# Kernel tuning notes

Hardware: AMD Instinct MI355X
Metric: run time of the kernel (lower is better)

Reference implementation:

```python
import jax, jax.numpy as jnp
from jax import lax
import numpy as np

B, L1, L2 = 64, 1024, 1024


def setup_inputs() -> dict:
    key = jax.random.key(0)
    ks = jax.random.split(key, 6)
    s1 = 1.0 / np.sqrt(L1)
    s2 = 1.0 / np.sqrt(L2)
    return {
        "a": jax.random.normal(ks[0], (B, L1), dtype=jnp.float32),
        "b": jax.random.normal(ks[1], (B, L2), dtype=jnp.float32),
        # nn.Linear(L1, L1) and nn.Linear(L2, L2) params (PyTorch default uniform init range)
        "W1": jax.random.uniform(ks[2], (L1, L1), jnp.float32, -s1, s1),
        "b1": jax.random.uniform(ks[3], (L1,), jnp.float32, -s1, s1),
        "W2": jax.random.uniform(ks[4], (L2, L2), jnp.float32, -s2, s2),
        "b2": jax.random.uniform(ks[5], (L2,), jnp.float32, -s2, s2),
    }


def _dtw_cost(cost):
    """DTW accumulated-cost DP for one [N, M] pairwise-cost matrix.

    R[i,j] = cost[i,j] + min(R[i-1,j-1], R[i-1,j], R[i,j-1]).
    The within-row dependency x[j] = c[j] + min(m[j], x[j-1]) is a min-plus
    prefix: x[j] = S[j] + cummin(m - S_{j-1}) with S = cumsum(c), which lets
    each row be computed in parallel (wavefront-equivalent vectorization).
    Returns the scalar DTW distance R[N-1, M-1].
    """
    dt = cost.dtype
    row0 = jnp.cumsum(cost[0])  # R[0, :]

    def step(prev_row, c_row):
        # m[j] = min(R[i-1, j], R[i-1, j-1]);  j=0 has no (i-1, j-1) neighbor
        shifted = jnp.concatenate([jnp.full((1,), jnp.inf, dt), prev_row[:-1]])
        m = jnp.minimum(prev_row, shifted)
        S = jnp.cumsum(c_row)
        S_prev = jnp.concatenate([jnp.zeros((1,), dt), S[:-1]])
        row = S + lax.associative_scan(jnp.minimum, m - S_prev)
        return row, None

    last_row, _ = lax.scan(step, row0, cost[1:])
    return last_row[-1]


def reference(a, b, W1, b1, W2, b2):
    # seq1 / seq2 linear projections over the time axis
    a_p = a @ W1.T + b1  # [B, L1]
    b_p = b @ W2.T + b2  # [B, L2]
    # squared-euclidean pairwise cost (scipy.sqeuclidean on scalar elements)
    cost = (a_p[:, :, None] - b_p[:, None, :]) ** 2  # [B, L1, L2]
    return jax.vmap(_dtw_cost)(cost)  # [B] DTW distances
```

## Files before the change

kernel.cpp:

```cpp
#include <hip/hip_runtime.h>
#include <math.h>


#define L 1024
#define BATCH 64

__global__ __launch_bounds__(256) void proj_kernel(
    const float* __restrict__ a, const float* __restrict__ b,
    const float* __restrict__ W1, const float* __restrict__ b1,
    const float* __restrict__ W2, const float* __restrict__ b2,
    float* __restrict__ ap, float* __restrict__ bp, int KC) {
  int part = blockIdx.x >> 7;
  int sub = blockIdx.x & 127;
  const float* X;
  const float* W;
  const float* bias;
  float* out;
  int i0;
  if (sub < 64) {
    X = a; W = W1; bias = b1; out = ap + part * BATCH * L; i0 = sub * 16;
  } else {
    X = b; W = W2; bias = b2; out = bp + part * BATCH * L; i0 = (sub - 64) * 16;
  }

  __shared__ float a_s[64][33];
  __shared__ float w_s[16][33];

  int tid = threadIdx.x;
  int lane_b = tid & 63;
  int iq = tid >> 6;

  float acc[4] = {0.f, 0.f, 0.f, 0.f};

  int kbeg = part * KC;
  int kend = kbeg + KC;
  for (int k0 = kbeg; k0 < kend; k0 += 32) {
    {
      int row = tid >> 2;
      int kl = (tid & 3) * 8;
      const float4* src = reinterpret_cast<const float4*>(&X[row * L + k0 + kl]);
      float4 v0 = src[0];
      float4 v1 = src[1];
      a_s[row][kl + 0] = v0.x; a_s[row][kl + 1] = v0.y;
      a_s[row][kl + 2] = v0.z; a_s[row][kl + 3] = v0.w;
      a_s[row][kl + 4] = v1.x; a_s[row][kl + 5] = v1.y;
      a_s[row][kl + 6] = v1.z; a_s[row][kl + 7] = v1.w;
    }
    {
      int row = tid >> 4;
      int kl = (tid & 15) * 2;
      float2 v = *reinterpret_cast<const float2*>(&W[(i0 + row) * L + k0 + kl]);
      w_s[row][kl] = v.x;
      w_s[row][kl + 1] = v.y;
    }
    __syncthreads();
    #pragma unroll 8
    for (int kl = 0; kl < 32; ++kl) {
      float av = a_s[lane_b][kl];
      #pragma unroll
      for (int m = 0; m < 4; ++m) {
        acc[m] += av * w_s[iq * 4 + m][kl];
      }
    }
    __syncthreads();
  }

  #pragma unroll
  for (int m = 0; m < 4; ++m) {
    int i = i0 + iq * 4 + m;
    float bv = (part == 0) ? bias[i] : 0.f;
    out[lane_b * L + i] = acc[m] + bv;
  }
}


#define NW 4
#define CPL 4
#define KBAR 32
#define OFF 95
#define DMAX (OFF * (NW - 1) + 63)
#define NG 43
#define NSTEPS (NG * KBAR)
#define APPAD (DMAX + NSTEPS + 64)

__device__ __forceinline__ float dpp_shr1(float v, float old) {
  int r = __builtin_amdgcn_update_dpp(__float_as_int(old), __float_as_int(v),
                                      0x138, 0xf, 0xf, false);
  return __int_as_float(r);
}

__device__ __forceinline__ float dpp_shl1(float v) {
  int r = __builtin_amdgcn_update_dpp(__float_as_int(v), __float_as_int(v),
                                      0x130, 0xf, 0xf, false);
  return __int_as_float(r);
}

__device__ __forceinline__ float min3f(float x, float y, float z) {
  float r;
  asm("v_min3_f32 %0, %1, %2, %3" : "=v"(r) : "v"(x), "v"(y), "v"(z));
  return r;
}

__global__ __launch_bounds__(256) void dtw_kernel(const float* __restrict__ app,
                                                  const float* __restrict__ bpp,
                                                  float* __restrict__ out,
                                                  int parts) {
  const int b = blockIdx.x;
  const int tid = threadIdx.x;
  const int w = tid >> 6;
  const int t = tid & 63;
  const int woff = w * OFF;
  const int D = woff + t;
  const float INF = INFINITY;

  __shared__ float ap_pad[APPAD];
  __shared__ float ring[NW - 1][64];

  for (int idx = tid; idx < APPAD; idx += 256) {
    int src = idx - DMAX;
    float v = 0.f;
    if ((unsigned)src < (unsigned)L) {
      v = app[b * L + src];
      for (int p = 1; p < parts; ++p) v += app[p * BATCH * L + b * L + src];
    }
    ap_pad[idx] = v;
  }

  float4 bv = *reinterpret_cast<const float4*>(&bpp[b * L + tid * CPL]);
  for (int p = 1; p < parts; ++p) {
    float4 u = *reinterpret_cast<const float4*>(
        &bpp[p * BATCH * L + b * L + tid * CPL]);
    bv.x += u.x; bv.y += u.y; bv.z += u.z; bv.w += u.w;
  }
  const float bpv0 = bv.x, bpv1 = bv.y, bpv2 = bv.z, bpv3 = bv.w;

  float p0 = INF, p1 = INF, p2 = INF, p3 = INF;
  float right = INF, prev_left = INF, apv = 0.f;
  float ringchunk = (w == 0 && t == 0) ? 0.f : INF;
  float apchunk = 0.f;
  float vprod = INF;
  const int ap_base = DMAX - woff + t;

  __syncthreads();

#define STEP_CORE()                                                          \
    float dprev = prev_left;                                                 \
    prev_left = left;                                                        \
    float d0 = apv - bpv0, d1 = apv - bpv1, d2 = apv - bpv2, d3 = apv - bpv3;\
    float x = left, bb;                                                      \
    bb = min3f(p0, dprev, x); x = __builtin_fmaf(d0, d0, bb); dprev = p0; p0 = x; \
    bb = min3f(p1, dprev, x); x = __builtin_fmaf(d1, d1, bb); dprev = p1; p1 = x; \
    bb = min3f(p2, dprev, x); x = __builtin_fmaf(d2, d2, bb); dprev = p2; p2 = x; \
    bb = min3f(p3, dprev, x); x = __builtin_fmaf(d3, d3, bb); p3 = x;        \
    right = x;

#define STEP_FAST()                                                          \
  {                                                                          \
    float left = dpp_shr1(right, ringchunk);                                 \
    apv = dpp_shr1(apv, apchunk);                                            \
    apchunk = dpp_shl1(apchunk);                                             \
    ringchunk = dpp_shl1(ringchunk);                                         \
    STEP_CORE();                                                             \
    vprod = dpp_shl1(vprod);                                                 \
    vprod = (t == 63) ? right : vprod;                                       \
  }

#define STEP_PRED(s)                                                         \
  {                                                                          \
    float left = dpp_shr1(right, ringchunk);                                 \
    apv = dpp_shr1(apv, apchunk);                                            \
    apchunk = dpp_shl1(apchunk);                                             \
    ringchunk = dpp_shl1(ringchunk);                                         \
    int ii = (s) - D;                                                        \
    if ((unsigned)ii < (unsigned)L) {                                        \
      STEP_CORE();                                                           \
    }                                                                        \
    vprod = dpp_shl1(vprod);                                                 \
    vprod = (t == 63) ? right : vprod;                                       \
  }

#define GROUP_LOAD(s0)                                                       \
    apchunk = ap_pad[ap_base + (s0)];                                        \
    if (w > 0 && t < KBAR)                                                   \
      ringchunk = ring[w - 1][((s0) - woff + t) & 63];

#define GROUP_STORE(s0)                                                      \
    if (w < NW - 1 && t >= 64 - KBAR)                                        \
      ring[w][((s0) - woff - 95 + t) & 63] = vprod;                          \
    __syncthreads();

  for (int g = 0; g < 11; ++g) {
    int s0 = g * KBAR;
    GROUP_LOAD(s0);
    #pragma unroll
    for (int k = 0; k < KBAR; ++k) STEP_PRED(s0 + k);
    GROUP_STORE(s0);
  }
  for (int g = 11; g < 32; ++g) {
    int s0 = g * KBAR;
    GROUP_LOAD(s0);
    #pragma unroll
    for (int k = 0; k < KBAR; ++k) STEP_FAST();
    GROUP_STORE(s0);
  }
  for (int g = 32; g < NG; ++g) {
    int s0 = g * KBAR;
    GROUP_LOAD(s0);
    #pragma unroll
    for (int k = 0; k < KBAR; ++k) STEP_PRED(s0 + k);
    GROUP_STORE(s0);
  }
#undef STEP_CORE
#undef STEP_FAST
#undef STEP_PRED
#undef GROUP_LOAD
#undef GROUP_STORE

  if (tid == NW * 64 - 1) out[b] = right;
}

extern "C" void kernel_launch(void* const* d_in, const int* in_sizes, int n_in,
                              void* d_out, int out_size, void* d_ws, size_t ws_size,
                              hipStream_t stream) {
  const float* a  = (const float*)d_in[0];
  const float* b  = (const float*)d_in[1];
  const float* W1 = (const float*)d_in[2];
  const float* b1 = (const float*)d_in[3];
  const float* W2 = (const float*)d_in[4];
  const float* b2 = (const float*)d_in[5];
  float* out = (float*)d_out;

  size_t per_part = (size_t)2 * BATCH * L * sizeof(float);
  int parts = 1;
  if (ws_size >= 4 * per_part) parts = 4;
  else if (ws_size >= 2 * per_part) parts = 2;

  float* ap = (float*)d_ws;
  float* bp = ap + (size_t)parts * BATCH * L;

  proj_kernel<<<128 * parts, 256, 0, stream>>>(a, b, W1, b1, W2, b2,
                                               ap, bp, L / parts);
  dtw_kernel<<<BATCH, 256, 0, stream>>>(ap, bp, out, parts);
}
```

Baseline: 99.79 us.

## Widen DTW wavefront to 8 waves and read projection weights directly

The DTW kernel now uses 8 wavefronts of 64 lanes with 2 columns per lane instead of 4 waves with 4 columns, which shortens the serial min-plus chain per step. The cost is more anti-diagonal groups (55 instead of 43), more barriers, and a longer predicated prologue. Separately, the projection kernel drops the shared-memory staging of W and reads W through wave-uniform scalar loads via readfirstlane, removing one LDS store path. The risk is that scalar memory latency for W is exposed in the inner loop.

```diff
diff --git a/kernel.cpp b/kernel.cpp
--- a/kernel.cpp
+++ b/kernel.cpp
@@ -24,11 +24,11 @@
   }
 
   __shared__ float a_s[64][33];
-  __shared__ float w_s[16][33];
 
   int tid = threadIdx.x;
   int lane_b = tid & 63;
-  int iq = tid >> 6;
+  int iq = __builtin_amdgcn_readfirstlane(tid >> 6);
+  const float* Wq = W + (size_t)(i0 + iq * 4) * L;
 
   float acc[4] = {0.f, 0.f, 0.f, 0.f};
 
@@ -46,20 +46,13 @@
       a_s[row][kl + 4] = v1.x; a_s[row][kl + 5] = v1.y;
       a_s[row][kl + 6] = v1.z; a_s[row][kl + 7] = v1.w;
     }
-    {
-      int row = tid >> 4;
-      int kl = (tid & 15) * 2;
-      float2 v = *reinterpret_cast<const float2*>(&W[(i0 + row) * L + k0 + kl]);
-      w_s[row][kl] = v.x;
-      w_s[row][kl + 1] = v.y;
-    }
     __syncthreads();
     #pragma unroll 8
     for (int kl = 0; kl < 32; ++kl) {
       float av = a_s[lane_b][kl];
       #pragma unroll
       for (int m = 0; m < 4; ++m) {
-        acc[m] += av * w_s[iq * 4 + m][kl];
+        acc[m] += av * Wq[m * L + k0 + kl];
       }
     }
     __syncthreads();
@@ -74,12 +67,12 @@
 }
 
 
-#define NW 4
-#define CPL 4
+#define NW 8
+#define CPL 2
 #define KBAR 32
 #define OFF 95
 #define DMAX (OFF * (NW - 1) + 63)
-#define NG 43
+#define NG 55
 #define NSTEPS (NG * KBAR)
 #define APPAD (DMAX + NSTEPS + 64)
 
@@ -101,7 +94,7 @@
   return r;
 }
 
-__global__ __launch_bounds__(256) void dtw_kernel(const float* __restrict__ app,
+__global__ __launch_bounds__(512) void dtw_kernel(const float* __restrict__ app,
                                                   const float* __restrict__ bpp,
                                                   float* __restrict__ out,
                                                   int parts) {
@@ -116,7 +109,7 @@
   __shared__ float ap_pad[APPAD];
   __shared__ float ring[NW - 1][64];
 
-  for (int idx = tid; idx < APPAD; idx += 256) {
+  for (int idx = tid; idx < APPAD; idx += 512) {
     int src = idx - DMAX;
     float v = 0.f;
     if ((unsigned)src < (unsigned)L) {
@@ -126,15 +119,15 @@
     ap_pad[idx] = v;
   }
 
-  float4 bv = *reinterpret_cast<const float4*>(&bpp[b * L + tid * CPL]);
+  float2 bv = *reinterpret_cast<const float2*>(&bpp[b * L + tid * CPL]);
   for (int p = 1; p < parts; ++p) {
-    float4 u = *reinterpret_cast<const float4*>(
+    float2 u = *reinterpret_cast<const float2*>(
         &bpp[p * BATCH * L + b * L + tid * CPL]);
-    bv.x += u.x; bv.y += u.y; bv.z += u.z; bv.w += u.w;
-  }
-  const float bpv0 = bv.x, bpv1 = bv.y, bpv2 = bv.z, bpv3 = bv.w;
-
-  float p0 = INF, p1 = INF, p2 = INF, p3 = INF;
+    bv.x += u.x; bv.y += u.y;
+  }
+  const float bpv0 = bv.x, bpv1 = bv.y;
+
+  float p0 = INF, p1 = INF;
   float right = INF, prev_left = INF, apv = 0.f;
   float ringchunk = (w == 0 && t == 0) ? 0.f : INF;
   float apchunk = 0.f;
@@ -146,12 +139,10 @@
 #define STEP_CORE()                                                          \
     float dprev = prev_left;                                                 \
     prev_left = left;                                                        \
-    float d0 = apv - bpv0, d1 = apv - bpv1, d2 = apv - bpv2, d3 = apv - bpv3;\
+    float d0 = apv - bpv0, d1 = apv - bpv1;                                  \
     float x = left, bb;                                                      \
     bb = min3f(p0, dprev, x); x = __builtin_fmaf(d0, d0, bb); dprev = p0; p0 = x; \
-    bb = min3f(p1, dprev, x); x = __builtin_fmaf(d1, d1, bb); dprev = p1; p1 = x; \
-    bb = min3f(p2, dprev, x); x = __builtin_fmaf(d2, d2, bb); dprev = p2; p2 = x; \
-    bb = min3f(p3, dprev, x); x = __builtin_fmaf(d3, d3, bb); p3 = x;        \
+    bb = min3f(p1, dprev, x); x = __builtin_fmaf(d1, d1, bb); p1 = x;        \
     right = x;
 
 #define STEP_FAST()                                                          \
@@ -186,17 +177,17 @@
 
 #define GROUP_STORE(s0)                                                      \
     if (w < NW - 1 && t >= 64 - KBAR)                                        \
-      ring[w][((s0) - woff - 95 + t) & 63] = vprod;                          \
+      ring[w][((s0) - woff - (63 + KBAR) + t) & 63] = vprod;                 \
     __syncthreads();
 
-  for (int g = 0; g < 11; ++g) {
+  for (int g = 0; g < 23; ++g) {
     int s0 = g * KBAR;
     GROUP_LOAD(s0);
     #pragma unroll
     for (int k = 0; k < KBAR; ++k) STEP_PRED(s0 + k);
     GROUP_STORE(s0);
   }
-  for (int g = 11; g < 32; ++g) {
+  for (int g = 23; g < 32; ++g) {
     int s0 = g * KBAR;
     GROUP_LOAD(s0);
     #pragma unroll
@@ -240,5 +231,5 @@
 
   proj_kernel<<<128 * parts, 256, 0, stream>>>(a, b, W1, b1, W2, b2,
                                                ap, bp, L / parts);
-  dtw_kernel<<<BATCH, 256, 0, stream>>>(ap, bp, out, parts);
-}
+  dtw_kernel<<<BATCH, 512, 0, stream>>>(ap, bp, out, parts);
+}
```

Result: slower. 144.7 us (+45.0%).
